# Optimization experiments

Measured on AMD Instinct MI355X. Metric: run time of the kernel, lower is better.

Reference implementation:

```python
import jax, jax.numpy as jnp
import numpy as np

N = 128          # vector size = 8*8*2
KAPPA = 0.276


def dd_opt(x, U):
    """Wilson-Dirac-style U(1) stencil operator (stand-in for external DDOpt).
    x: (B_or_1, C, 8, 8, 2) complex64 (lattice axes 2,3), U: (B, 2, 8, 8) complex64 links.
    D x = x - kappa * sum_mu [ U_mu(n) x(n+mu) + conj(U_mu(n-mu)) x(n-mu) ].
    """
    U0 = U[:, None, 0, :, :, None]  # (B,1,8,8,1) links in lattice dir 0 (axis 2)
    U1 = U[:, None, 1, :, :, None]  # links in lattice dir 1 (axis 3)
    hop = (U0 * jnp.roll(x, -1, axis=2)
           + jnp.conj(jnp.roll(U0, 1, axis=2)) * jnp.roll(x, 1, axis=2)
           + U1 * jnp.roll(x, -1, axis=3)
           + jnp.conj(jnp.roll(U1, 1, axis=3)) * jnp.roll(x, 1, axis=3))
    return x - KAPPA * hop


def setup_inputs() -> dict:
    key = jax.random.key(0)
    k1, k2 = jax.random.split(key)
    B = 1024
    n_entries = N * (N + 1) // 2  # 8256 lower-triangular entries
    net_out = jax.random.normal(k1, (B, n_entries), jnp.float32) * 0.1
    U1 = jax.random.uniform(k2, (B, 2, 8, 8), jnp.float32) * (2.0 * np.pi)  # link angles
    return {"net_out": net_out, "U1": U1}


def reference(net_out, U1):
    B = net_out.shape[0]
    r, c = np.tril_indices(N)
    # Lower-triangular factor L: (B, N, N) complex64
    L = jnp.zeros((B, N, N), jnp.complex64).at[:, r, c].set(net_out.astype(jnp.complex64))
    links = jnp.exp(1j * U1).astype(jnp.complex64)  # (B, 2, 8, 8) unit-modulus U(1) links

    # mat_vect(e_i) = L @ DD(L^H e_i); column i of L^H is conj(row i of L).
    # Apply DD to all 128 columns at once (columns stacked along axis 1).
    cols = jnp.conj(L).reshape(B, N, 8, 8, 2)        # cols[b, i] = L^H e_i
    y = dd_opt(cols, links).reshape(B, N, N)          # y[b, i] = DD(L^H e_i)
    diag = jnp.einsum('bik,bik->bi', L, y)            # (L y_i)_i  -> diagonal of L DD L^H
    trace = jnp.sum(diag.real, axis=1)                # trace_mat(U1, mat_vect)

    # trace2 = trace of DD itself: apply DD to identity columns.
    eye = jnp.eye(N, dtype=jnp.complex64).reshape(1, N, 8, 8, 2)
    y2 = dd_opt(eye, links).reshape(B, N, N)          # y2[b, i] = DD(e_i)
    trace2 = jnp.sum(jnp.diagonal(y2, axis1=1, axis2=2).real, axis=1)

    return jnp.mean(trace / trace2)
```

## Files before the change

### kernel.cpp

```cpp
#include <hip/hip_runtime.h>

#define KAPPA 0.276f
#define NTRI 8256
#define BATCH 1024
#define SCALE (1.0f / (128.0f * 1024.0f))

__device__ __forceinline__ float rotl2(float v) {
    return __int_as_float(__builtin_amdgcn_mov_dpp(__float_as_int(v),
                                                   0x12E, 0xF, 0xF, false));
}

__global__ __launch_bounds__(512) void trace_kernel(const float* __restrict__ net_out,
                                                    const float* __restrict__ U1,
                                                    float* __restrict__ ws) {
    const int bid = blockIdx.x;
    const int xcd = bid & 7;
    const int b   = (xcd << 7) + (bid >> 3);
    const int tid = threadIdx.x;
    const int w   = tid >> 6;
    const int l   = tid & 63;
    const int r   = w;

    const float* __restrict__ X = net_out + (size_t)b * NTRI;
    const float* __restrict__ U = U1 + (size_t)b * 128;

    const float m2k = -2.0f * KAPPA;
    const float cAl = m2k * __cosf(U[(l >> 1)]);
    const float cAh = m2k * __cosf(U[32 + (l >> 1)]);
    const float cBl = m2k * __cosf(U[64 + (l >> 1)]);
    const float cBh = m2k * __cosf(U[96 + (l >> 1)]);

    const int  sidx = (l + 16) & 63;
    const bool lo48 = (l < 48);

    float sq = 0.f, hAl = 0.f, hBl = 0.f, hAh = 0.f, hBh = 0.f;

    {
        int i = r;
        int o = (r * (r + 1)) >> 1;
        #pragma unroll 4
        for (int t = 0; t < 8; ++t) {
            const float* __restrict__ R = X + o;
            float x = R[l];
            x = (l <= i) ? x : 0.f;
            float ash = __shfl(x, sidx, 64);
            float a   = lo48 ? ash : 0.f;
            float bb  = rotl2(x);
            sq  = fmaf(x, x,  sq);
            hAl = fmaf(x, a,  hAl);
            hBl = fmaf(x, bb, hBl);
            o += (i << 3) + 36;
            i += 8;
        }
    }
    {
        int i = r + 64;
        int o = (i * (i + 1)) >> 1;
        #pragma unroll 4
        for (int t = 0; t < 8; ++t) {
            const float* __restrict__ R = X + o;
            float x  = R[l];
            float xh = R[l + 64];
            xh = (l + 64 <= i) ? xh : 0.f;

            float sx  = __shfl(x,  sidx, 64);
            float sxh = __shfl(xh, sidx, 64);
            float a   = lo48 ? sx  : sxh;
            float ah  = lo48 ? sxh : sx;

            float bb = rotl2(x);
            float bh = rotl2(xh);

            sq  = fmaf(x,  x,  sq);
            sq  = fmaf(xh, xh, sq);
            hAl = fmaf(x,  a,  hAl);
            hBl = fmaf(x,  bb, hBl);
            hAh = fmaf(xh, ah, hAh);
            hBh = fmaf(xh, bh, hBh);

            o += (i << 3) + 36;
            i += 8;
        }
    }

    float val = sq + cAl * hAl + cAh * hAh + cBl * hBl + cBh * hBh;

    #pragma unroll
    for (int off = 32; off > 0; off >>= 1)
        val += __shfl_down(val, off, 64);

    __shared__ float red[8];
    if (l == 0) red[w] = val;
    __syncthreads();
    if (tid == 0) {
        float p = 0.f;
        #pragma unroll
        for (int j = 0; j < 8; ++j) p += red[j];
        ws[bid] = p;
    }
}

__global__ __launch_bounds__(1024) void reduce_kernel(const float* __restrict__ ws,
                                                      float* __restrict__ out) {
    const int tid = threadIdx.x;
    float v = ws[tid];
    #pragma unroll
    for (int off = 32; off > 0; off >>= 1)
        v += __shfl_down(v, off, 64);
    __shared__ float red[16];
    if ((tid & 63) == 0) red[tid >> 6] = v;
    __syncthreads();
    if (tid < 64) {
        float s = (tid < 16) ? red[tid] : 0.f;
        #pragma unroll
        for (int off = 8; off > 0; off >>= 1)
            s += __shfl_down(s, off, 64);
        if (tid == 0) out[0] = s * SCALE;
    }
}

extern "C" void kernel_launch(void* const* d_in, const int* in_sizes, int n_in,
                              void* d_out, int out_size, void* d_ws, size_t ws_size,
                              hipStream_t stream) {
    const float* net_out = (const float*)d_in[0];
    const float* U1      = (const float*)d_in[1];
    float* out = (float*)d_out;
    float* ws  = (float*)d_ws;

    trace_kernel<<<BATCH, 512, 0, stream>>>(net_out, U1, ws);
    reduce_kernel<<<1, 1024, 0, stream>>>(ws, out);
}
```

Before: 12.29 us.

## Restructure row traversal into float4 loads with DPP row shifts

Each lane now handles four consecutive columns via float4 loads, and each wave's 16-lane groups process four rows per pass instead of a serial eight-row loop per wave. The neighbour terms are formed with DPP row-rotate and quad-permute moves in place of the ds_bpermute-based __shfl. This is meant to cut the number of load instructions and the cross-lane shuffle latency, and to expose more memory-level parallelism by issuing all loads up front. In exchange it does more cos evaluations per lane, raises register pressure, and relies on the float4 row offsets being 16-byte aligned, which the triangular row starts may not be.

```diff
diff --git a/kernel.cpp b/kernel.cpp
--- a/kernel.cpp
+++ b/kernel.cpp
@@ -5,9 +5,11 @@
 #define BATCH 1024
 #define SCALE (1.0f / (128.0f * 1024.0f))
 
-__device__ __forceinline__ float rotl2(float v) {
-    return __int_as_float(__builtin_amdgcn_mov_dpp(__float_as_int(v),
-                                                   0x12E, 0xF, 0xF, false));
+__device__ __forceinline__ float ror4(float v) {
+    return __int_as_float(__builtin_amdgcn_mov_dpp(__float_as_int(v), 0x12C, 0xF, 0xF, false));
+}
+__device__ __forceinline__ float qp1(float v) {
+    return __int_as_float(__builtin_amdgcn_mov_dpp(__float_as_int(v), 0x39, 0xF, 0xF, false));
 }
 
 __global__ __launch_bounds__(512) void trace_kernel(const float* __restrict__ net_out,
@@ -19,71 +21,102 @@
     const int tid = threadIdx.x;
     const int w   = tid >> 6;
     const int l   = tid & 63;
-    const int r   = w;
+    const int m   = l & 15;
+    const int g   = l >> 4;
 
     const float* __restrict__ X = net_out + (size_t)b * NTRI;
     const float* __restrict__ U = U1 + (size_t)b * 128;
 
-    const float m2k = -2.0f * KAPPA;
-    const float cAl = m2k * __cosf(U[(l >> 1)]);
-    const float cAh = m2k * __cosf(U[32 + (l >> 1)]);
-    const float cBl = m2k * __cosf(U[64 + (l >> 1)]);
-    const float cBh = m2k * __cosf(U[96 + (l >> 1)]);
+    const int r0 = w + (g << 3);
+    const int r1 = r0 + 32;
+    const int r2 = r0 + 64;
+    const int r3 = r0 + 96;
+    const int t0 = (r0 * (r0 + 1)) >> 1;
+    const int t1 = (r1 * (r1 + 1)) >> 1;
+    const int t2 = (r2 * (r2 + 1)) >> 1;
+    const int t3 = (r3 * (r3 + 1)) >> 1;
+    const int c0 = m << 2;
 
-    const int  sidx = (l + 16) & 63;
-    const bool lo48 = (l < 48);
+    const float4 L1  = *(const float4*)(X + t0 + c0);
+    const float4 L2  = *(const float4*)(X + t1 + c0);
+    const float4 H1P = *(const float4*)(X + t2 + c0);
+    const float4 H1Q = *(const float4*)(X + t2 + 64 + c0);
+    const float4 H2P = *(const float4*)(X + t3 + c0);
+    const float4 H2Q = *(const float4*)(X + t3 + 64 + c0);
 
-    float sq = 0.f, hAl = 0.f, hBl = 0.f, hAh = 0.f, hBh = 0.f;
+    const bool mlt12 = (m < 12);
+
+    float sq = 0.f;
+    float hAp01 = 0.f, hAp23 = 0.f, hAq01 = 0.f, hAq23 = 0.f;
+    float hBp01 = 0.f, hBp23 = 0.f, hBq01 = 0.f, hBq23 = 0.f;
 
     {
-        int i = r;
-        int o = (r * (r + 1)) >> 1;
-        #pragma unroll 4
-        for (int t = 0; t < 8; ++t) {
-            const float* __restrict__ R = X + o;
-            float x = R[l];
-            x = (l <= i) ? x : 0.f;
-            float ash = __shfl(x, sidx, 64);
-            float a   = lo48 ? ash : 0.f;
-            float bb  = rotl2(x);
-            sq  = fmaf(x, x,  sq);
-            hAl = fmaf(x, a,  hAl);
-            hBl = fmaf(x, bb, hBl);
-            o += (i << 3) + 36;
-            i += 8;
-        }
-    }
-    {
-        int i = r + 64;
-        int o = (i * (i + 1)) >> 1;
-        #pragma unroll 4
-        for (int t = 0; t < 8; ++t) {
-            const float* __restrict__ R = X + o;
-            float x  = R[l];
-            float xh = R[l + 64];
-            xh = (l + 64 <= i) ? xh : 0.f;
-
-            float sx  = __shfl(x,  sidx, 64);
-            float sxh = __shfl(xh, sidx, 64);
-            float a   = lo48 ? sx  : sxh;
-            float ah  = lo48 ? sxh : sx;
-
-            float bb = rotl2(x);
-            float bh = rotl2(xh);
-
-            sq  = fmaf(x,  x,  sq);
-            sq  = fmaf(xh, xh, sq);
-            hAl = fmaf(x,  a,  hAl);
-            hBl = fmaf(x,  bb, hBl);
-            hAh = fmaf(xh, ah, hAh);
-            hBh = fmaf(xh, bh, hBh);
-
-            o += (i << 3) + 36;
-            i += 8;
-        }
+        float x0 = (c0     <= r0) ? L1.x : 0.f;
+        float x1 = (c0 + 1 <= r0) ? L1.y : 0.f;
+        float x2 = (c0 + 2 <= r0) ? L1.z : 0.f;
+        float x3 = (c0 + 3 <= r0) ? L1.w : 0.f;
+        float a0 = mlt12 ? ror4(x0) : 0.f;
+        float a1 = mlt12 ? ror4(x1) : 0.f;
+        float a2 = mlt12 ? ror4(x2) : 0.f;
+        float a3 = mlt12 ? ror4(x3) : 0.f;
+        sq    += x0*x0 + x1*x1 + x2*x2 + x3*x3;
+        hAp01 = fmaf(x0, a0, fmaf(x1, a1, hAp01));
+        hAp23 = fmaf(x2, a2, fmaf(x3, a3, hAp23));
+        hBp01 = fmaf(x0, x2, fmaf(x1, x3, hBp01));
+        hBp23 = fmaf(x2, qp1(x0), fmaf(x3, qp1(x1), hBp23));
+        float y0 = (c0     <= r1) ? L2.x : 0.f;
+        float y1 = (c0 + 1 <= r1) ? L2.y : 0.f;
+        float y2 = (c0 + 2 <= r1) ? L2.z : 0.f;
+        float y3 = (c0 + 3 <= r1) ? L2.w : 0.f;
+        float e0 = mlt12 ? ror4(y0) : 0.f;
+        float e1 = mlt12 ? ror4(y1) : 0.f;
+        float e2 = mlt12 ? ror4(y2) : 0.f;
+        float e3 = mlt12 ? ror4(y3) : 0.f;
+        sq    += y0*y0 + y1*y1 + y2*y2 + y3*y3;
+        hAp01 = fmaf(y0, e0, fmaf(y1, e1, hAp01));
+        hAp23 = fmaf(y2, e2, fmaf(y3, e3, hAp23));
+        hBp01 = fmaf(y0, y2, fmaf(y1, y3, hBp01));
+        hBp23 = fmaf(y2, qp1(y0), fmaf(y3, qp1(y1), hBp23));
     }
 
-    float val = sq + cAl * hAl + cAh * hAh + cBl * hBl + cBh * hBh;
+    #pragma unroll
+    for (int s = 0; s < 2; ++s) {
+        const int   i  = s ? r3 : r2;
+        const float4 P = s ? H2P : H1P;
+        const float4 Q = s ? H2Q : H1Q;
+        const int   cq = c0 + 64;
+        float p0 = P.x, p1 = P.y, p2 = P.z, p3 = P.w;
+        float q0 = (cq     <= i) ? Q.x : 0.f;
+        float q1 = (cq + 1 <= i) ? Q.y : 0.f;
+        float q2 = (cq + 2 <= i) ? Q.z : 0.f;
+        float q3 = (cq + 3 <= i) ? Q.w : 0.f;
+
+        float rp0 = ror4(p0), rp1 = ror4(p1), rp2 = ror4(p2), rp3 = ror4(p3);
+        float rq0 = ror4(q0), rq1 = ror4(q1), rq2 = ror4(q2), rq3 = ror4(q3);
+        float aP0 = mlt12 ? rp0 : rq0, aP1 = mlt12 ? rp1 : rq1;
+        float aP2 = mlt12 ? rp2 : rq2, aP3 = mlt12 ? rp3 : rq3;
+        float aQ0 = mlt12 ? rq0 : rp0, aQ1 = mlt12 ? rq1 : rp1;
+        float aQ2 = mlt12 ? rq2 : rp2, aQ3 = mlt12 ? rq3 : rp3;
+
+        sq += p0*p0 + p1*p1 + p2*p2 + p3*p3;
+        sq += q0*q0 + q1*q1 + q2*q2 + q3*q3;
+        hAp01 = fmaf(p0, aP0, fmaf(p1, aP1, hAp01));
+        hAp23 = fmaf(p2, aP2, fmaf(p3, aP3, hAp23));
+        hAq01 = fmaf(q0, aQ0, fmaf(q1, aQ1, hAq01));
+        hAq23 = fmaf(q2, aQ2, fmaf(q3, aQ3, hAq23));
+        hBp01 = fmaf(p0, p2, fmaf(p1, p3, hBp01));
+        hBp23 = fmaf(p2, qp1(p0), fmaf(p3, qp1(p1), hBp23));
+        hBq01 = fmaf(q0, q2, fmaf(q1, q3, hBq01));
+        hBq23 = fmaf(q2, qp1(q0), fmaf(q3, qp1(q1), hBq23));
+    }
+
+    const float m2k = -2.0f * KAPPA;
+    const int   m2  = m << 1;
+    float hop = __cosf(U[m2])      * hAp01 + __cosf(U[m2 + 1])      * hAp23
+              + __cosf(U[32 + m2]) * hAq01 + __cosf(U[32 + m2 + 1]) * hAq23
+              + __cosf(U[64 + m2]) * hBp01 + __cosf(U[64 + m2 + 1]) * hBp23
+              + __cosf(U[96 + m2]) * hBq01 + __cosf(U[96 + m2 + 1]) * hBq23;
+    float val = fmaf(m2k, hop, sq);
 
     #pragma unroll
     for (int off = 32; off > 0; off >>= 1)
```

New measurement: 11.76 us. -4.3%, faster.
